# Performance work log

Measured on AMD Instinct MI355X. Metric: run time of the kernel, lower is better.

The kernel has to match this reference:

```python
import jax, jax.numpy as jnp
import numpy as np

NEG = -1e30  # log-space 'zero'
EPS = 1e-7   # matches keras ctc_batch_cost log(y_pred + epsilon)


def _lse3(a, b, c):
    x = jnp.stack([a, b, c], axis=0)
    m = jnp.max(x, axis=0)
    return m + jnp.log(jnp.sum(jnp.exp(x - m), axis=0))


def ctc_batch_cost(y_true, y_pred):
    # y_true: [B, U] int labels in [0, C-1); y_pred: [B, T, C] probabilities.
    # Blank = C-1 (Keras/TF convention). Full input_length=T, label_length=U.
    B, T, C = y_pred.shape
    U = y_true.shape[1]
    blank = C - 1
    S = 2 * U + 1

    logp = jnp.log(y_pred + EPS)  # [B, T, C]

    # extended label sequence: blank, l1, blank, l2, ..., blank  -> [B, S]
    ext = jnp.full((B, S), blank, dtype=y_true.dtype)
    ext = ext.at[:, 1::2].set(y_true)

    # gather per-timestep log-probs of extended labels: [B, T, S] -> [T, B, S]
    lp_ext = jnp.take_along_axis(logp, ext[:, None, :].astype(jnp.int32), axis=2)
    lp_ext = jnp.transpose(lp_ext, (1, 0, 2))

    # skip-transition allowed where ext[s] != blank and ext[s] != ext[s-2]
    shifted = jnp.concatenate(
        [jnp.full((B, 2), -1, dtype=ext.dtype), ext[:, :-2]], axis=1)
    allow_skip = (ext != blank) & (ext != shifted)  # [B, S]

    # alpha init at t=0: only s=0 (blank) and s=1 (first label) are reachable
    s_idx = jnp.arange(S)
    alpha0 = jnp.where(s_idx[None, :] < 2, lp_ext[0], NEG)  # [B, S]

    pad1 = jnp.full((B, 1), NEG, dtype=logp.dtype)
    pad2 = jnp.full((B, 2), NEG, dtype=logp.dtype)

    def step(alpha, lp_t):
        a1 = jnp.concatenate([pad1, alpha[:, :-1]], axis=1)
        a2 = jnp.concatenate([pad2, alpha[:, :-2]], axis=1)
        a2 = jnp.where(allow_skip, a2, NEG)
        new = _lse3(alpha, a1, a2) + lp_t
        return new, None

    alpha_T, _ = jax.lax.scan(step, alpha0, lp_ext[1:])

    # total path log-prob ends at last blank or last label
    m = jnp.maximum(alpha_T[:, -1], alpha_T[:, -2])
    ll = m + jnp.log(jnp.exp(alpha_T[:, -1] - m) + jnp.exp(alpha_T[:, -2] - m))
    return -ll[:, None]  # [B, 1], matching keras ctc_batch_cost


def setup_inputs() -> dict:
    key = jax.random.key(0)
    k1, k2 = jax.random.split(key)
    B, T, C, U = 256, 512, 128, 48
    # post-softmax frame probabilities, as the layer expects
    y_pred = jax.nn.softmax(jax.random.normal(k1, (B, T, C), dtype=jnp.float32), axis=-1)
    y_true = jax.random.randint(k2, (B, U), 0, C - 1, dtype=jnp.int64)
    return {"y_true": y_true, "y_pred": y_pred}


def reference(y_true, y_pred):
    return ctc_batch_cost(y_true, y_pred)
```

## Files before the change

### kernel.cpp

```cpp
#include <hip/hip_runtime.h>

#define T_STEPS 512
#define C_CH    128
#define U_LAB   48
#define PF      16
#define NEGF    (-1e30f)
#define EPSF    (1e-7f)

#define SB0() __builtin_amdgcn_sched_barrier(0)

__device__ __forceinline__ float fexp2(float x) {
#if __has_builtin(__builtin_amdgcn_exp2f)
    return __builtin_amdgcn_exp2f(x);
#else
    return __builtin_exp2f(x);
#endif
}
__device__ __forceinline__ float flog2(float x) {
#if __has_builtin(__builtin_amdgcn_logf)
    return __builtin_amdgcn_logf(x);
#else
    return __builtin_log2f(x);
#endif
}

__device__ __forceinline__ float dpp_shr1_negfill(float x) {
    int r = __builtin_amdgcn_update_dpp(__builtin_bit_cast(int, NEGF),
                                        __builtin_bit_cast(int, x),
                                        0x138, 0xF, 0xF, false);
    return __builtin_bit_cast(float, r);
}
__device__ __forceinline__ float dpp_shl1_negfill(float x) {
    int r = __builtin_amdgcn_update_dpp(__builtin_bit_cast(int, NEGF),
                                        __builtin_bit_cast(int, x),
                                        0x130, 0xF, 0xF, false);
    return __builtin_bit_cast(float, r);
}

__device__ __forceinline__ float lse2f(float x, float y) {
    float m = fmaxf(x, y);
    float d = -fabsf(x - y);
    return m + flog2(1.0f + fexp2(d));
}

__global__ __launch_bounds__(128) void ctc_mitm_kernel(const int* __restrict__ yt,
                                                       const float* __restrict__ yp,
                                                       float* __restrict__ out) {
    __shared__ float s_fa0[64];
    __shared__ float s_fa1[64];

    const int b    = blockIdx.x;
    const int lane = threadIdx.x & 63;
    const int wav  = threadIdx.x >> 6;

    const bool is_lab = (lane < U_LAB);
    const int  lab    = is_lab ? yt[b * U_LAB + lane] : 0;
    const float* __restrict__ base = yp + (size_t)b * T_STEPS * C_CH;
    const float* pB = base + (C_CH - 1);
    const float* pL = base + lab;

    float a0, a1;
    float lpb255 = 0.0f, lpl255 = 0.0f;

    if (wav == 0) {
        int labprev = __builtin_amdgcn_update_dpp(-1, lab, 0x138, 0xF, 0xF, false);
        const bool allow = (lane >= 1) && is_lab && (lab != labprev);

        {
            float pb = base[C_CH - 1];
            float pl = base[lab];
            a0 = (lane == 0) ? flog2(pb + EPSF) : NEGF;
            a1 = (lane == 0) ? flog2(pl + EPSF) : NEGF;
        }

        float curB[PF], curL[PF];
#pragma unroll
        for (int k = 0; k < PF; ++k) {
            curB[k] = pB[(size_t)(1 + k) * C_CH];
            curL[k] = pL[(size_t)(1 + k) * C_CH];
        }
        SB0();

        int t0 = 1;
#pragma unroll 1
        for (int body = 0; body < 15; ++body) {
#pragma unroll
            for (int k = 0; k < PF; ++k) {
                float lpb = flog2(curB[k] + EPSF);
                float lpl = flog2(curL[k] + EPSF);
                float p1  = dpp_shr1_negfill(a1);
                float n0  = lse2f(a0, p1) + lpb;
                float c2  = allow ? p1 : NEGF;
                float m1  = fmaxf(fmaxf(a1, a0), c2);
                float n1  = m1 + flog2(fexp2(a1 - m1) + fexp2(a0 - m1) + fexp2(c2 - m1)) + lpl;
                a0 = n0; a1 = n1;
                curB[k] = pB[(size_t)(t0 + k + PF) * C_CH];
                curL[k] = pL[(size_t)(t0 + k + PF) * C_CH];
                SB0();
            }
            t0 += PF;
        }
#pragma unroll
        for (int k = 0; k < PF - 1; ++k) {
            float lpb = flog2(curB[k] + EPSF);
            float lpl = flog2(curL[k] + EPSF);
            float p1  = dpp_shr1_negfill(a1);
            float n0  = lse2f(a0, p1) + lpb;
            float c2  = allow ? p1 : NEGF;
            float m1  = fmaxf(fmaxf(a1, a0), c2);
            float n1  = m1 + flog2(fexp2(a1 - m1) + fexp2(a0 - m1) + fexp2(c2 - m1)) + lpl;
            a0 = n0; a1 = n1;
        }
        s_fa0[lane] = a0;
        s_fa1[lane] = a1;
    } else {
        int labnext = (lane + 1 < U_LAB) ? yt[b * U_LAB + lane + 1] : -1;
        const bool allowD = (lane + 1 < U_LAB) && (lab != labnext);

        {
            const float* row = base + (size_t)(T_STEPS - 1) * C_CH;
            float pb = row[C_CH - 1];
            float pl = row[lab];
            a0 = (lane == 48) ? flog2(pb + EPSF) : NEGF;
            a1 = (lane == 47) ? flog2(pl + EPSF) : NEGF;
        }

        float curB[PF], curL[PF];
#pragma unroll
        for (int k = 0; k < PF; ++k) {
            curB[k] = pB[(size_t)(510 - k) * C_CH];
            curL[k] = pL[(size_t)(510 - k) * C_CH];
        }
        SB0();

        int t0 = 510;
#pragma unroll 1
        for (int body = 0; body < 16; ++body) {
#pragma unroll
            for (int k = 0; k < PF; ++k) {
                float lpb = flog2(curB[k] + EPSF);
                float lpl = flog2(curL[k] + EPSF);
                float b0  = dpp_shl1_negfill(a0);
                float b1  = dpp_shl1_negfill(a1);
                float n0  = lse2f(a0, a1) + lpb;
                float c2  = allowD ? b1 : NEGF;
                float m1  = fmaxf(fmaxf(a1, b0), c2);
                float n1  = m1 + flog2(fexp2(a1 - m1) + fexp2(b0 - m1) + fexp2(c2 - m1)) + lpl;
                a0 = n0; a1 = n1;
                if (body == 15 && k == PF - 1) { lpb255 = lpb; lpl255 = lpl; }
                curB[k] = pB[(size_t)(t0 - k - PF) * C_CH];
                curL[k] = pL[(size_t)(t0 - k - PF) * C_CH];
                SB0();
            }
            t0 -= PF;
        }
    }

    __syncthreads();

    if (wav == 1) {
        float c0 = s_fa0[lane] + a0 - lpb255;
        float c1 = s_fa1[lane] + a1 - lpl255;
        float c  = lse2f(c0, c1);
#pragma unroll
        for (int off = 32; off >= 1; off >>= 1)
            c = lse2f(c, __shfl_xor(c, off));
        if (lane == 0) out[b] = -(c * 0.69314718055994530942f);
    }
}

extern "C" void kernel_launch(void* const* d_in, const int* in_sizes, int n_in,
                              void* d_out, int out_size, void* d_ws, size_t ws_size,
                              hipStream_t stream) {
    const int*   yt  = (const int*)d_in[0];
    const float* yp  = (const float*)d_in[1];
    float*       out = (float*)d_out;
    const int B = in_sizes[0] / U_LAB;
    ctc_mitm_kernel<<<B, 128, 0, stream>>>(yt, yp, out);
}
```

Before: 27.70 us.

## Replace log-space CTC recursion with exponent-rescaled linear-space forward and backward passes

Each wave now runs the full CTC recursion in linear probability space, using plain adds and multiplies instead of exp2/log2 log-sum-exp. Underflow is avoided by rescaling alpha every four steps with a power-of-two factor taken from a wave-wide max, and the exponent shift is tracked in an integer. The meet-in-the-middle split and shared-memory combine are gone. Wave 0 runs the full forward pass and wave 1 the full backward pass, and the block parity picks which result is written, so each wave walks twice as many timesteps and one wave's result is discarded. The aim is a much shorter per-step dependency chain with no transcendentals, at the cost of the longer sequential chain, twice the loads per wave and the cross-lane reduction for rescaling.

```diff
diff --git a/kernel.cpp b/kernel.cpp
--- a/kernel.cpp
+++ b/kernel.cpp
@@ -4,18 +4,9 @@
 #define C_CH    128
 #define U_LAB   48
 #define PF      16
-#define NEGF    (-1e30f)
 #define EPSF    (1e-7f)
-
 #define SB0() __builtin_amdgcn_sched_barrier(0)
 
-__device__ __forceinline__ float fexp2(float x) {
-#if __has_builtin(__builtin_amdgcn_exp2f)
-    return __builtin_amdgcn_exp2f(x);
-#else
-    return __builtin_exp2f(x);
-#endif
-}
 __device__ __forceinline__ float flog2(float x) {
 #if __has_builtin(__builtin_amdgcn_logf)
     return __builtin_amdgcn_logf(x);
@@ -24,31 +15,42 @@
 #endif
 }
 
-__device__ __forceinline__ float dpp_shr1_negfill(float x) {
-    int r = __builtin_amdgcn_update_dpp(__builtin_bit_cast(int, NEGF),
-                                        __builtin_bit_cast(int, x),
-                                        0x138, 0xF, 0xF, false);
-    return __builtin_bit_cast(float, r);
-}
-__device__ __forceinline__ float dpp_shl1_negfill(float x) {
-    int r = __builtin_amdgcn_update_dpp(__builtin_bit_cast(int, NEGF),
-                                        __builtin_bit_cast(int, x),
-                                        0x130, 0xF, 0xF, false);
+template <int CTRL>
+__device__ __forceinline__ float dpp0(float x) {
+    int r = __builtin_amdgcn_update_dpp(0, __builtin_bit_cast(int, x),
+                                        CTRL, 0xF, 0xF, false);
     return __builtin_bit_cast(float, r);
 }
 
-__device__ __forceinline__ float lse2f(float x, float y) {
-    float m = fmaxf(x, y);
-    float d = -fabsf(x - y);
-    return m + flog2(1.0f + fexp2(d));
+__device__ __forceinline__ float rdlane(float x, int l) {
+    return __builtin_bit_cast(float, __builtin_amdgcn_readlane(__builtin_bit_cast(int, x), l));
 }
 
-__global__ __launch_bounds__(128) void ctc_mitm_kernel(const int* __restrict__ yt,
-                                                       const float* __restrict__ yp,
-                                                       float* __restrict__ out) {
-    __shared__ float s_fa0[64];
-    __shared__ float s_fa1[64];
+__device__ __forceinline__ float wave_max4(float v) {
+    float mx = v;
+    mx = fmaxf(mx, dpp0<0x111>(mx));
+    mx = fmaxf(mx, dpp0<0x112>(mx));
+    mx = fmaxf(mx, dpp0<0x114>(mx));
+    mx = fmaxf(mx, dpp0<0x118>(mx));
+    float m01 = fmaxf(rdlane(mx, 15), rdlane(mx, 31));
+    float m23 = fmaxf(rdlane(mx, 47), rdlane(mx, 63));
+    return fmaxf(m01, m23);
+}
 
+template <int TGT_FIELD>
+__device__ __forceinline__ void rescale2(float& a0, float& a1, int& cum) {
+    float m  = wave_max4(fmaxf(a0, a1));
+    int   E  = (__builtin_bit_cast(int, m) >> 23) & 0xFF;
+    int   f  = TGT_FIELD + 127 - E;
+    f = (f < 1) ? 1 : (f > 254 ? 254 : f);
+    cum -= f - 127;
+    float sc = __builtin_bit_cast(float, f << 23);
+    a0 *= sc; a1 *= sc;
+}
+
+__global__ __launch_bounds__(128) void ctc_bisect_kernel(const int* __restrict__ yt,
+                                                         const float* __restrict__ yp,
+                                                         float* __restrict__ out) {
     const int b    = blockIdx.x;
     const int lane = threadIdx.x & 63;
     const int wav  = threadIdx.x >> 6;
@@ -60,18 +62,19 @@
     const float* pL = base + lab;
 
     float a0, a1;
-    float lpb255 = 0.0f, lpl255 = 0.0f;
+    int   cum = 0;
 
     if (wav == 0) {
         int labprev = __builtin_amdgcn_update_dpp(-1, lab, 0x138, 0xF, 0xF, false);
         const bool allow = (lane >= 1) && is_lab && (lab != labprev);
 
         {
-            float pb = base[C_CH - 1];
-            float pl = base[lab];
-            a0 = (lane == 0) ? flog2(pb + EPSF) : NEGF;
-            a1 = (lane == 0) ? flog2(pl + EPSF) : NEGF;
+            float pb0 = base[C_CH - 1] + EPSF;
+            float pl0 = base[lab] + EPSF;
+            a0 = (lane == 0) ? pb0 : 0.0f;
+            a1 = (lane == 0) ? pl0 : 0.0f;
         }
+        rescale2<190>(a0, a1, cum);
 
         float curB[PF], curL[PF];
 #pragma unroll
@@ -81,49 +84,54 @@
         }
         SB0();
 
+#define FWD_STEP(k)  do { \
+            float pb2 = curB[k] + EPSF; \
+            float pl2 = is_lab ? (curL[k] + EPSF) : 0.0f; \
+            float p1  = dpp0<0x138>(a1);                  \
+            float s3  = a1 + a0 + (allow ? p1 : 0.0f); \
+            a0 = (a0 + p1) * pb2; \
+            a1 = s3 * pl2; \
+        } while (0)
+
         int t0 = 1;
 #pragma unroll 1
-        for (int body = 0; body < 15; ++body) {
+        for (int body = 0; body < 31; ++body) {
 #pragma unroll
             for (int k = 0; k < PF; ++k) {
-                float lpb = flog2(curB[k] + EPSF);
-                float lpl = flog2(curL[k] + EPSF);
-                float p1  = dpp_shr1_negfill(a1);
-                float n0  = lse2f(a0, p1) + lpb;
-                float c2  = allow ? p1 : NEGF;
-                float m1  = fmaxf(fmaxf(a1, a0), c2);
-                float n1  = m1 + flog2(fexp2(a1 - m1) + fexp2(a0 - m1) + fexp2(c2 - m1)) + lpl;
-                a0 = n0; a1 = n1;
-                curB[k] = pB[(size_t)(t0 + k + PF) * C_CH];
-                curL[k] = pL[(size_t)(t0 + k + PF) * C_CH];
+                FWD_STEP(k);
+                int tn = t0 + k + PF; tn = (tn < T_STEPS - 1) ? tn : (T_STEPS - 1);
+                curB[k] = pB[(size_t)tn * C_CH];
+                curL[k] = pL[(size_t)tn * C_CH];
                 SB0();
+                if ((k & 3) == 3) rescale2<190>(a0, a1, cum);
             }
             t0 += PF;
         }
 #pragma unroll
         for (int k = 0; k < PF - 1; ++k) {
-            float lpb = flog2(curB[k] + EPSF);
-            float lpl = flog2(curL[k] + EPSF);
-            float p1  = dpp_shr1_negfill(a1);
-            float n0  = lse2f(a0, p1) + lpb;
-            float c2  = allow ? p1 : NEGF;
-            float m1  = fmaxf(fmaxf(a1, a0), c2);
-            float n1  = m1 + flog2(fexp2(a1 - m1) + fexp2(a0 - m1) + fexp2(c2 - m1)) + lpl;
-            a0 = n0; a1 = n1;
+            FWD_STEP(k);
+            if ((k & 3) == 3) rescale2<190>(a0, a1, cum);
         }
-        s_fa0[lane] = a0;
-        s_fa1[lane] = a1;
+
+        float v96 = __shfl(a0, 48);
+        float v95 = __shfl(a1, 47);
+        float ll2 = flog2(v95 + v96) + (float)cum;
+        if (((b & 1) == 0) && lane == 0)
+            out[b] = -(ll2 * 0.69314718055994530942f);
+        else
+            asm volatile("" :: "v"(ll2));
     } else {
         int labnext = (lane + 1 < U_LAB) ? yt[b * U_LAB + lane + 1] : -1;
         const bool allowD = (lane + 1 < U_LAB) && (lab != labnext);
 
         {
             const float* row = base + (size_t)(T_STEPS - 1) * C_CH;
-            float pb = row[C_CH - 1];
-            float pl = row[lab];
-            a0 = (lane == 48) ? flog2(pb + EPSF) : NEGF;
-            a1 = (lane == 47) ? flog2(pl + EPSF) : NEGF;
+            float pb0 = row[C_CH - 1] + EPSF;
+            float pl0 = row[lab] + EPSF;
+            a0 = (lane == 48) ? pb0 : 0.0f;
+            a1 = (lane == 47) ? pl0 : 0.0f;
         }
+        rescale2<190>(a0, a1, cum);
 
         float curB[PF], curL[PF];
 #pragma unroll
@@ -133,39 +141,43 @@
         }
         SB0();
 
+#define BWD_STEP(k)  do { \
+            float pb2 = curB[k] + EPSF; \
+            float pl2 = is_lab ? (curL[k] + EPSF) : 0.0f; \
+            float b0  = dpp0<0x130>(a0);                  \
+            float b1  = dpp0<0x130>(a1);                  \
+            float s3  = a1 + b0 + (allowD ? b1 : 0.0f); \
+            a0 = (a0 + a1) * pb2; \
+            a1 = s3 * pl2; \
+        } while (0)
+
         int t0 = 510;
 #pragma unroll 1
-        for (int body = 0; body < 16; ++body) {
+        for (int body = 0; body < 31; ++body) {
 #pragma unroll
             for (int k = 0; k < PF; ++k) {
-                float lpb = flog2(curB[k] + EPSF);
-                float lpl = flog2(curL[k] + EPSF);
-                float b0  = dpp_shl1_negfill(a0);
-                float b1  = dpp_shl1_negfill(a1);
-                float n0  = lse2f(a0, a1) + lpb;
-                float c2  = allowD ? b1 : NEGF;
-                float m1  = fmaxf(fmaxf(a1, b0), c2);
-                float n1  = m1 + flog2(fexp2(a1 - m1) + fexp2(b0 - m1) + fexp2(c2 - m1)) + lpl;
-                a0 = n0; a1 = n1;
-                if (body == 15 && k == PF - 1) { lpb255 = lpb; lpl255 = lpl; }
-                curB[k] = pB[(size_t)(t0 - k - PF) * C_CH];
-                curL[k] = pL[(size_t)(t0 - k - PF) * C_CH];
+                BWD_STEP(k);
+                int tn = t0 - k - PF; tn = (tn > 0) ? tn : 0;
+                curB[k] = pB[(size_t)tn * C_CH];
+                curL[k] = pL[(size_t)tn * C_CH];
                 SB0();
+                if ((k & 3) == 3) rescale2<190>(a0, a1, cum);
             }
             t0 -= PF;
         }
-    }
+#pragma unroll
+        for (int k = 0; k < PF - 1; ++k) {
+            BWD_STEP(k);
+            if ((k & 3) == 3) rescale2<190>(a0, a1, cum);
+        }
 
-    __syncthreads();
-
-    if (wav == 1) {
-        float c0 = s_fa0[lane] + a0 - lpb255;
-        float c1 = s_fa1[lane] + a1 - lpl255;
-        float c  = lse2f(c0, c1);
-#pragma unroll
-        for (int off = 32; off >= 1; off >>= 1)
-            c = lse2f(c, __shfl_xor(c, off));
-        if (lane == 0) out[b] = -(c * 0.69314718055994530942f);
+        float w0 = __shfl(a0, 0);
+        float w1 = __shfl(a1, 0);
+        float ll2 = flog2(w0 + w1) + (float)cum;
+        if (((b & 1) == 1) && lane == 0)
+            out[b] = -(ll2 * 0.69314718055994530942f);
+        else
+            asm volatile("" :: "v"(ll2));
     }
 }
 
@@ -176,5 +188,5 @@
     const float* yp  = (const float*)d_in[1];
     float*       out = (float*)d_out;
     const int B = in_sizes[0] / U_LAB;
-    ctc_mitm_kernel<<<B, 128, 0, stream>>>(yt, yp, out);
+    ctc_bisect_kernel<<<B, 128, 0, stream>>>(yt, yp, out);
 }
```

Result: slower. 38.62 us (+39.4%).
